# Kernel optimization log

Hardware: AMD Instinct MI355X
Metric: run time of the kernel (lower is better)

The kernel has to match this reference:

```python
import jax, jax.numpy as jnp
import numpy as np

NUM_GRAPHS = 64


def gcn_conv(x, W, b, row, col, ew, n_nodes):
    # PyG GCNConv with edge weights: add self-loops (weight 1), symmetric norm.
    deg = jax.ops.segment_sum(ew, col, num_segments=n_nodes) + 1.0  # self-loop weight
    dis = jnp.where(deg > 0, jax.lax.rsqrt(deg), 0.0)
    norm = dis[row] * ew * dis[col]  # [E]
    xw = x @ W  # [N, H]
    # edge messages aggregated at target (col) + self-loop contribution dis_i^2 * xw_i
    agg = jnp.zeros_like(xw).at[col].add(norm[:, None] * xw[row])
    agg = agg + (dis * dis)[:, None] * xw
    return agg + b


def reference(x, edge_index, edge_attr, batch, W1, b1, W2, b2, actor_w, actor_b, critic_w, critic_b):
    n_nodes = x.shape[0]
    row, col = edge_index[0], edge_index[1]
    ew = jnp.abs(edge_attr)
    h = jax.nn.relu(gcn_conv(x, W1, b1, row, col, ew, n_nodes))
    # dropout p=0.1 is identity in eval mode
    h = jax.nn.relu(gcn_conv(h, W2, b2, row, col, ew, n_nodes))
    action_logits = (h @ actor_w + actor_b)[:, 0]  # [N]
    # global mean pool over graphs
    sums = jax.ops.segment_sum(h, batch, num_segments=NUM_GRAPHS)  # [G, H]
    counts = jax.ops.segment_sum(jnp.ones((n_nodes,), h.dtype), batch, num_segments=NUM_GRAPHS)
    graph_embed = sums / jnp.maximum(counts, 1.0)[:, None]
    value = graph_embed @ critic_w + critic_b  # [G, 1]
    return (action_logits, value)


def setup_inputs() -> dict:
    key = jax.random.key(0)
    ks = jax.random.split(key, 10)
    N, F, H, E = 100000, 128, 64, 1600000
    s = lambda fan: 1.0 / np.sqrt(fan)
    return {
        "x": jax.random.normal(ks[0], (N, F), jnp.float32),
        "edge_index": jax.random.randint(ks[1], (2, E), 0, N, jnp.int32),
        "edge_attr": jax.random.normal(ks[2], (E,), jnp.float32),
        "batch": jnp.sort(jax.random.randint(ks[3], (N,), 0, 64, jnp.int32)),
        "W1": jax.random.normal(ks[4], (F, H), jnp.float32) * s(F),
        "b1": jnp.zeros((H,), jnp.float32),
        "W2": jax.random.normal(ks[5], (H, H), jnp.float32) * s(H),
        "b2": jnp.zeros((H,), jnp.float32),
        "actor_w": jax.random.normal(ks[6], (H, 1), jnp.float32) * s(H),
        "actor_b": jnp.zeros((1,), jnp.float32),
        "critic_w": jax.random.normal(ks[7], (H, 1), jnp.float32) * s(H),
        "critic_b": jnp.zeros((1,), jnp.float32),
    }
```

## Files before the change

kernel.cpp:

```cpp
#include <hip/hip_runtime.h>
#include <hip/hip_fp16.h>


#define TB 256
#define BSH2 9
#define BW2 512
#define CHUNK 4096
#define NB1MAX 256

__global__ __launch_bounds__(256) void passA_k(const int* __restrict__ col,
                                               const int* __restrict__ row,
                                               const float* __restrict__ ea,
                                               int* __restrict__ gCur,
                                               uint2* __restrict__ recA,
                                               int E, int CAPB, int NB1) {
    __shared__ int hist[NB1MAX], base[NB1MAX], cur[NB1MAX];
    int t = threadIdx.x;
    int e0 = blockIdx.x * CHUNK;
    if (t < NB1MAX) { hist[t] = 0; cur[t] = 0; }
    __syncthreads();
    for (int i = t; i < CHUNK; i += 256) {
        int e = e0 + i;
        if (e < E) atomicAdd(&hist[col[e] >> BSH2], 1);
    }
    __syncthreads();
    if (t < NB1) base[t] = atomicAdd(&gCur[t], hist[t]);
    __syncthreads();
    for (int i = t; i < CHUNK; i += 256) {
        int e = e0 + i;
        if (e >= E) continue;
        int c = col[e];
        int b = c >> BSH2;
        int pos = base[b] + atomicAdd(&cur[b], 1);
        if (pos < CAPB)
            recA[(size_t)b * CAPB + pos] =
                make_uint2(((unsigned)(c & (BW2 - 1)) << 17) | (unsigned)row[e],
                           __float_as_uint(fabsf(ea[e])));
    }
}

__global__ __launch_bounds__(256) void passB_k(const int* __restrict__ gCur,
                                               const uint2* __restrict__ recA,
                                               uint2* __restrict__ rec,
                                               int* __restrict__ ptr,
                                               int* __restrict__ cnt,
                                               float* __restrict__ dis,
                                               int N, int CAPB) {
    __shared__ int hist[BW2], excl[BW2], cur[BW2];
    __shared__ float sumL[BW2];
    __shared__ int part[256];
    int b = blockIdx.x, t = threadIdx.x;
    int nrec = min(gCur[b], CAPB);
    for (int i = t; i < BW2; i += 256) { hist[i] = 0; cur[i] = 0; sumL[i] = 0.f; }
    __syncthreads();
    const uint2* ra = recA + (size_t)b * CAPB;
    for (int i = t; i < nrec; i += 256) {
        uint2 r = ra[i];
        int lc = r.x >> 17;
        atomicAdd(&hist[lc], 1);
        atomicAdd(&sumL[lc], __uint_as_float(r.y));
    }
    __syncthreads();
    int s0 = hist[t * 2], s = s0 + hist[t * 2 + 1];
    part[t] = s;
    __syncthreads();
    for (int d = 1; d < 256; d <<= 1) {
        int v = (t >= d) ? part[t - d] : 0;
        __syncthreads();
        part[t] += v;
        __syncthreads();
    }
    int poff = t ? part[t - 1] : 0;
    excl[t * 2] = poff;
    excl[t * 2 + 1] = poff + s0;
    __syncthreads();
    for (int i = t; i < nrec; i += 256) {
        uint2 r = ra[i];
        int lc = r.x >> 17;
        int pos = atomicAdd(&cur[lc], 1);
        rec[(size_t)b * CAPB + excl[lc] + pos] = make_uint2(r.x & 0x1FFFFu, r.y);
    }
    int c0 = b << BSH2;
    for (int i = t; i < BW2; i += 256) {
        int node = c0 + i;
        if (node < N) {
            ptr[node] = b * CAPB + excl[i];
            cnt[node] = hist[i];
            dis[node] = rsqrtf(sumL[i] + 1.0f);
        }
    }
}

template <int K>
__global__ __launch_bounds__(256) void gemm_k(const float* __restrict__ X,
                                              const float* __restrict__ W,
                                              __half* __restrict__ Y, int N) {
    __shared__ float xs[16 * K];
    const int tid = threadIdx.x;
    const int row0 = blockIdx.x * 16;
    const float4* X4 = reinterpret_cast<const float4*>(X + (size_t)row0 * K);
    float4* xs4 = reinterpret_cast<float4*>(xs);
    for (int idx = tid; idx < 16 * K / 4; idx += 256) {
        int r = row0 + (idx * 4) / K;
        xs4[idx] = (r < N) ? X4[idx] : float4{0.f, 0.f, 0.f, 0.f};
    }
    __syncthreads();
    const int c  = tid & 63;
    const int rg = tid >> 6;
    const float4* xp0 = reinterpret_cast<const float4*>(xs + (rg * 4 + 0) * K);
    const float4* xp1 = reinterpret_cast<const float4*>(xs + (rg * 4 + 1) * K);
    const float4* xp2 = reinterpret_cast<const float4*>(xs + (rg * 4 + 2) * K);
    const float4* xp3 = reinterpret_cast<const float4*>(xs + (rg * 4 + 3) * K);
    float a0 = 0.f, a1 = 0.f, a2 = 0.f, a3 = 0.f;
#pragma unroll 2
    for (int k4 = 0; k4 < K / 4; ++k4) {
        float4 x0 = xp0[k4], x1 = xp1[k4], x2 = xp2[k4], x3 = xp3[k4];
        const float* wp = W + k4 * 4 * 64 + c;
        float w0 = wp[0], w1 = wp[64], w2 = wp[128], w3 = wp[192];
        a0 = fmaf(x0.x, w0, a0); a0 = fmaf(x0.y, w1, a0);
        a0 = fmaf(x0.z, w2, a0); a0 = fmaf(x0.w, w3, a0);
        a1 = fmaf(x1.x, w0, a1); a1 = fmaf(x1.y, w1, a1);
        a1 = fmaf(x1.z, w2, a1); a1 = fmaf(x1.w, w3, a1);
        a2 = fmaf(x2.x, w0, a2); a2 = fmaf(x2.y, w1, a2);
        a2 = fmaf(x2.z, w2, a2); a2 = fmaf(x2.w, w3, a2);
        a3 = fmaf(x3.x, w0, a3); a3 = fmaf(x3.y, w1, a3);
        a3 = fmaf(x3.z, w2, a3); a3 = fmaf(x3.w, w3, a3);
    }
    int r = row0 + rg * 4;
    if (r < N)     Y[(size_t)r * 64 + c]       = __float2half(a0);
    if (r + 1 < N) Y[(size_t)(r + 1) * 64 + c] = __float2half(a1);
    if (r + 2 < N) Y[(size_t)(r + 2) * 64 + c] = __float2half(a2);
    if (r + 3 < N) Y[(size_t)(r + 3) * 64 + c] = __float2half(a3);
}

__global__ __launch_bounds__(256) void agg_fin_k(const int* __restrict__ ptr,
                                                 const int* __restrict__ cnt,
                                                 const uint2* __restrict__ rec,
                                                 const float* __restrict__ dis,
                                                 const __half2* __restrict__ xw2,
                                                 const float* __restrict__ bias,
                                                 float* __restrict__ h, int N) {
    int n = blockIdx.x * 4 + (threadIdx.x >> 6);
    if (n >= N) return;
    int lane = threadIdx.x & 63;
    int half_id = lane >> 5;
    int fl = lane & 31;
    int base = ptr[n], num = cnt[n];
    float ax = 0.f, ay = 0.f;
    for (int k0 = 0; k0 < num; k0 += 64) {
        int rem = min(num - k0, 64);
        int r = 0; float w = 0.f;
        if (lane < rem) {
            uint2 rv = rec[(size_t)base + k0 + lane];
            r = (int)rv.x;
            w = __uint_as_float(rv.y) * dis[r];
        }
        int k = 0;
        for (; k + 15 < rem; k += 16) {
            int i0 = k + half_id;
            int   ra0 = __shfl(r, i0),      ra1 = __shfl(r, i0 + 2);
            int   ra2 = __shfl(r, i0 + 4),  ra3 = __shfl(r, i0 + 6);
            int   ra4 = __shfl(r, i0 + 8),  ra5 = __shfl(r, i0 + 10);
            int   ra6 = __shfl(r, i0 + 12), ra7 = __shfl(r, i0 + 14);
            float wa0 = __shfl(w, i0),      wa1 = __shfl(w, i0 + 2);
            float wa2 = __shfl(w, i0 + 4),  wa3 = __shfl(w, i0 + 6);
            float wa4 = __shfl(w, i0 + 8),  wa5 = __shfl(w, i0 + 10);
            float wa6 = __shfl(w, i0 + 12), wa7 = __shfl(w, i0 + 14);
            __half2 v0 = xw2[(size_t)ra0 * 32 + fl];
            __half2 v1 = xw2[(size_t)ra1 * 32 + fl];
            __half2 v2 = xw2[(size_t)ra2 * 32 + fl];
            __half2 v3 = xw2[(size_t)ra3 * 32 + fl];
            __half2 v4 = xw2[(size_t)ra4 * 32 + fl];
            __half2 v5 = xw2[(size_t)ra5 * 32 + fl];
            __half2 v6 = xw2[(size_t)ra6 * 32 + fl];
            __half2 v7 = xw2[(size_t)ra7 * 32 + fl];
            float2 f;
            f = __half22float2(v0); ax = fmaf(wa0, f.x, ax); ay = fmaf(wa0, f.y, ay);
            f = __half22float2(v1); ax = fmaf(wa1, f.x, ax); ay = fmaf(wa1, f.y, ay);
            f = __half22float2(v2); ax = fmaf(wa2, f.x, ax); ay = fmaf(wa2, f.y, ay);
            f = __half22float2(v3); ax = fmaf(wa3, f.x, ax); ay = fmaf(wa3, f.y, ay);
            f = __half22float2(v4); ax = fmaf(wa4, f.x, ax); ay = fmaf(wa4, f.y, ay);
            f = __half22float2(v5); ax = fmaf(wa5, f.x, ax); ay = fmaf(wa5, f.y, ay);
            f = __half22float2(v6); ax = fmaf(wa6, f.x, ax); ay = fmaf(wa6, f.y, ay);
            f = __half22float2(v7); ax = fmaf(wa7, f.x, ax); ay = fmaf(wa7, f.y, ay);
        }
        for (; k + 1 < rem; k += 2) {
            int i = k + half_id;
            int ra = __shfl(r, i); float wa = __shfl(w, i);
            float2 f = __half22float2(xw2[(size_t)ra * 32 + fl]);
            ax = fmaf(wa, f.x, ax); ay = fmaf(wa, f.y, ay);
        }
        if (k < rem) {
            int ra = __shfl(r, k); float wa = __shfl(w, k);
            if (half_id == 0) {
                float2 f = __half22float2(xw2[(size_t)ra * 32 + fl]);
                ax = fmaf(wa, f.x, ax); ay = fmaf(wa, f.y, ay);
            }
        }
    }
    ax += __shfl(ax, lane ^ 32);
    ay += __shfl(ay, lane ^ 32);
    if (half_id == 0) {
        float d = dis[n];
        float2 xs = __half22float2(xw2[(size_t)n * 32 + fl]);
        float2 bb = reinterpret_cast<const float2*>(bias)[fl];
        float svx = fmaf(d, xs.x, ax);
        float svy = fmaf(d, xs.y, ay);
        float2 out;
        out.x = fmaxf(fmaf(d, svx, bb.x), 0.0f);
        out.y = fmaxf(fmaf(d, svy, bb.y), 0.0f);
        reinterpret_cast<float2*>(h)[(size_t)n * 32 + fl] = out;
    }
}

__global__ __launch_bounds__(256) void heads_k(const float* __restrict__ h,
                                               const float* __restrict__ aw,
                                               const float* __restrict__ ab,
                                               const int* __restrict__ batch,
                                               float* __restrict__ logits,
                                               float* __restrict__ sums,
                                               float* __restrict__ counts,
                                               int N, int C) {
    int wave = blockIdx.x * 4 + (threadIdx.x >> 6);
    int lane = threadIdx.x & 63;
    int start = wave * C;
    if (start >= N) return;
    int end = min(start + C, N);
    float aww = aw[lane];
    float abv = ab[0];
    int cur = batch[start];
    float acc = 0.f;
    int cntv = 0;
    for (int i = start; i < end; ++i) {
        float hv = h[(size_t)i * 64 + lane];
        float p = hv * aww;
        for (int off = 32; off; off >>= 1) p += __shfl_down(p, off);
        if (lane == 0) logits[i] = p + abv;
        int g = batch[i];
        if (g != cur) {
            atomicAdd(&sums[cur * 64 + lane], acc);
            if (lane == 0) atomicAdd(&counts[cur], (float)cntv);
            acc = 0.f; cntv = 0; cur = g;
        }
        acc += hv; ++cntv;
    }
    atomicAdd(&sums[cur * 64 + lane], acc);
    if (lane == 0) atomicAdd(&counts[cur], (float)cntv);
}

__global__ void value_k(const float* __restrict__ sums, const float* __restrict__ counts,
                        const float* __restrict__ cw, const float* __restrict__ cb,
                        float* __restrict__ val) {
    int g = blockIdx.x;
    int lane = threadIdx.x;
    float cntv = fmaxf(counts[g], 1.0f);
    float p = (sums[g * 64 + lane] / cntv) * cw[lane];
    for (int off = 32; off; off >>= 1) p += __shfl_down(p, off);
    if (lane == 0) val[g] = p + cb[0];
}

extern "C" void kernel_launch(void* const* d_in, const int* in_sizes, int n_in,
                              void* d_out, int out_size, void* d_ws, size_t ws_size,
                              hipStream_t stream) {
    const float* x     = (const float*)d_in[0];
    const int*   ei    = (const int*)d_in[1];
    const float* ea    = (const float*)d_in[2];
    const int*   batch = (const int*)d_in[3];
    const float* W1    = (const float*)d_in[4];
    const float* b1    = (const float*)d_in[5];
    const float* W2    = (const float*)d_in[6];
    const float* b2    = (const float*)d_in[7];
    const float* aw    = (const float*)d_in[8];
    const float* ab    = (const float*)d_in[9];
    const float* cw    = (const float*)d_in[10];
    const float* cb    = (const float*)d_in[11];

    const int N = in_sizes[3];
    const int E = in_sizes[2];
    const int H = 64, G = 64;
    const int* row = ei;
    const int* col = ei + E;

    const int NB1  = (N + BW2 - 1) >> BSH2;
    const int CAPB = (((E / NB1) * 5 / 4 + 256) + 1) & ~1;

    float*  dis    = (float*)d_ws;
    int*    gCur   = (int*)(dis + N);
    uint2*  recA   = (uint2*)(gCur + NB1MAX);
    uint2*  rec    = recA + (size_t)NB1 * CAPB;
    int*    ptr    = (int*)(rec + (size_t)NB1 * CAPB);
    int*    cnt    = ptr + N;
    __half* xwh    = (__half*)(cnt + N);
    float*  bufB   = (float*)(xwh + (size_t)N * H);
    float*  sums   = bufB + (size_t)N * H;
    float*  counts = sums + G * H;

    float* logits = (float*)d_out;
    float* value  = logits + N;

    hipMemsetAsync(gCur, 0, (size_t)NB1MAX * 4, stream);
    passA_k<<<(E + CHUNK - 1) / CHUNK, 256, 0, stream>>>(col, row, ea, gCur, recA, E, CAPB, NB1);
    passB_k<<<NB1, 256, 0, stream>>>(gCur, recA, rec, ptr, cnt, dis, N, CAPB);

    gemm_k<128><<<(N + 15) / 16, 256, 0, stream>>>(x, W1, xwh, N);
    agg_fin_k<<<(N + 3) / 4, 256, 0, stream>>>(ptr, cnt, rec, dis,
                                               (const __half2*)xwh, b1, bufB, N);

    gemm_k<64><<<(N + 15) / 16, 256, 0, stream>>>(bufB, W2, xwh, N);
    agg_fin_k<<<(N + 3) / 4, 256, 0, stream>>>(ptr, cnt, rec, dis,
                                               (const __half2*)xwh, b2, bufB, N);

    hipMemsetAsync(sums, 0, (size_t)(G * H + G) * 4, stream);
    const int WAVES = 4096;
    const int C = (N + WAVES - 1) / WAVES;
    heads_k<<<WAVES / 4, 256, 0, stream>>>(bufB, aw, ab, batch, logits, sums, counts, N, C);
    value_k<<<G, 64, 0, stream>>>(sums, counts, cw, cb, value);
}
```

Before: 274.0 us.

## Store hidden activations in fp16, fuse actor logits into aggregation, merge memsets

Hidden activations between layers are now stored as fp16 instead of fp32, halving the traffic for the layer-1 output, the layer-2 GEMM input and the pooling input. The actor-head dot product is computed inside the second aggregation kernel with a wave shuffle reduction, so the separate heads kernel becomes a pooling-only kernel working on half2 data. The two memsets are merged into one by moving sums, counts and the cursor array next to each other in the workspace. Rounding hidden activations to fp16 adds precision loss, and the fused logits use fp32 values that differ slightly from the rounded values used in pooling.

```diff
diff --git a/kernel.cpp b/kernel.cpp
--- a/kernel.cpp
+++ b/kernel.cpp
@@ -91,18 +91,30 @@
     }
 }
 
-template <int K>
-__global__ __launch_bounds__(256) void gemm_k(const float* __restrict__ X,
+template <int K, typename T>
+__global__ __launch_bounds__(256) void gemm_k(const T* __restrict__ X,
                                               const float* __restrict__ W,
                                               __half* __restrict__ Y, int N) {
     __shared__ float xs[16 * K];
     const int tid = threadIdx.x;
     const int row0 = blockIdx.x * 16;
-    const float4* X4 = reinterpret_cast<const float4*>(X + (size_t)row0 * K);
     float4* xs4 = reinterpret_cast<float4*>(xs);
-    for (int idx = tid; idx < 16 * K / 4; idx += 256) {
-        int r = row0 + (idx * 4) / K;
-        xs4[idx] = (r < N) ? X4[idx] : float4{0.f, 0.f, 0.f, 0.f};
+    if constexpr (sizeof(T) == 4) {
+        const float4* X4 = reinterpret_cast<const float4*>((const float*)X + (size_t)row0 * K);
+        for (int idx = tid; idx < 16 * K / 4; idx += 256) {
+            int r = row0 + (idx * 4) / K;
+            xs4[idx] = (r < N) ? X4[idx] : float4{0.f, 0.f, 0.f, 0.f};
+        }
+    } else {
+        const __half2* X2 = reinterpret_cast<const __half2*>((const __half*)X + (size_t)row0 * K);
+        for (int idx = tid; idx < 16 * K / 4; idx += 256) {
+            int r = row0 + (idx * 4) / K;
+            if (r < N) {
+                float2 fa = __half22float2(X2[2 * idx]);
+                float2 fb = __half22float2(X2[2 * idx + 1]);
+                xs4[idx] = float4{fa.x, fa.y, fb.x, fb.y};
+            } else xs4[idx] = float4{0.f, 0.f, 0.f, 0.f};
+        }
     }
     __syncthreads();
     const int c  = tid & 63;
@@ -133,13 +145,17 @@
     if (r + 3 < N) Y[(size_t)(r + 3) * 64 + c] = __float2half(a3);
 }
 
+template <bool WITH_LOGITS>
 __global__ __launch_bounds__(256) void agg_fin_k(const int* __restrict__ ptr,
                                                  const int* __restrict__ cnt,
                                                  const uint2* __restrict__ rec,
                                                  const float* __restrict__ dis,
                                                  const __half2* __restrict__ xw2,
                                                  const float* __restrict__ bias,
-                                                 float* __restrict__ h, int N) {
+                                                 __half2* __restrict__ hout,
+                                                 const float* __restrict__ aw,
+                                                 const float* __restrict__ ab,
+                                                 float* __restrict__ logits, int N) {
     int n = blockIdx.x * 4 + (threadIdx.x >> 6);
     if (n >= N) return;
     int lane = threadIdx.x & 63;
@@ -204,48 +220,52 @@
         float d = dis[n];
         float2 xs = __half22float2(xw2[(size_t)n * 32 + fl]);
         float2 bb = reinterpret_cast<const float2*>(bias)[fl];
-        float svx = fmaf(d, xs.x, ax);
-        float svy = fmaf(d, xs.y, ay);
         float2 out;
-        out.x = fmaxf(fmaf(d, svx, bb.x), 0.0f);
-        out.y = fmaxf(fmaf(d, svy, bb.y), 0.0f);
-        reinterpret_cast<float2*>(h)[(size_t)n * 32 + fl] = out;
-    }
-}
-
-__global__ __launch_bounds__(256) void heads_k(const float* __restrict__ h,
-                                               const float* __restrict__ aw,
-                                               const float* __restrict__ ab,
-                                               const int* __restrict__ batch,
-                                               float* __restrict__ logits,
-                                               float* __restrict__ sums,
-                                               float* __restrict__ counts,
-                                               int N, int C) {
+        out.x = fmaxf(fmaf(d, fmaf(d, xs.x, ax), bb.x), 0.0f);
+        out.y = fmaxf(fmaf(d, fmaf(d, xs.y, ay), bb.y), 0.0f);
+        hout[(size_t)n * 32 + fl] = __float22half2_rn(out);
+        if constexpr (WITH_LOGITS) {
+            float2 awv = reinterpret_cast<const float2*>(aw)[fl];
+            float lg = out.x * awv.x + out.y * awv.y;
+            lg += __shfl(lg, lane ^ 1);
+            lg += __shfl(lg, lane ^ 2);
+            lg += __shfl(lg, lane ^ 4);
+            lg += __shfl(lg, lane ^ 8);
+            lg += __shfl(lg, lane ^ 16);
+            if (lane == 0) logits[n] = lg + ab[0];
+        }
+    }
+}
+
+__global__ __launch_bounds__(256) void pool_k(const __half2* __restrict__ h2,
+                                              const int* __restrict__ batch,
+                                              float* __restrict__ sums,
+                                              float* __restrict__ counts,
+                                              int N, int C) {
     int wave = blockIdx.x * 4 + (threadIdx.x >> 6);
     int lane = threadIdx.x & 63;
     int start = wave * C;
     if (start >= N) return;
+    if (lane >= 32) return;
     int end = min(start + C, N);
-    float aww = aw[lane];
-    float abv = ab[0];
+    int fl = lane;
     int cur = batch[start];
-    float acc = 0.f;
+    float accx = 0.f, accy = 0.f;
     int cntv = 0;
     for (int i = start; i < end; ++i) {
-        float hv = h[(size_t)i * 64 + lane];
-        float p = hv * aww;
-        for (int off = 32; off; off >>= 1) p += __shfl_down(p, off);
-        if (lane == 0) logits[i] = p + abv;
+        float2 v = __half22float2(h2[(size_t)i * 32 + fl]);
         int g = batch[i];
         if (g != cur) {
-            atomicAdd(&sums[cur * 64 + lane], acc);
-            if (lane == 0) atomicAdd(&counts[cur], (float)cntv);
-            acc = 0.f; cntv = 0; cur = g;
-        }
-        acc += hv; ++cntv;
-    }
-    atomicAdd(&sums[cur * 64 + lane], acc);
-    if (lane == 0) atomicAdd(&counts[cur], (float)cntv);
+            atomicAdd(&sums[cur * 64 + 2 * fl], accx);
+            atomicAdd(&sums[cur * 64 + 2 * fl + 1], accy);
+            if (fl == 0) atomicAdd(&counts[cur], (float)cntv);
+            accx = 0.f; accy = 0.f; cntv = 0; cur = g;
+        }
+        accx += v.x; accy += v.y; ++cntv;
+    }
+    atomicAdd(&sums[cur * 64 + 2 * fl], accx);
+    atomicAdd(&sums[cur * 64 + 2 * fl + 1], accy);
+    if (fl == 0) atomicAdd(&counts[cur], (float)cntv);
 }
 
 __global__ void value_k(const float* __restrict__ sums, const float* __restrict__ counts,
@@ -284,35 +304,35 @@
     const int NB1  = (N + BW2 - 1) >> BSH2;
     const int CAPB = (((E / NB1) * 5 / 4 + 256) + 1) & ~1;
 
-    float*  dis    = (float*)d_ws;
-    int*    gCur   = (int*)(dis + N);
-    uint2*  recA   = (uint2*)(gCur + NB1MAX);
+    float*  sums   = (float*)d_ws;
+    float*  counts = sums + G * H;
+    int*    gCur   = (int*)(counts + G);
+    float*  dis    = (float*)(gCur + NB1MAX);
+    uint2*  recA   = (uint2*)(dis + N);
     uint2*  rec    = recA + (size_t)NB1 * CAPB;
     int*    ptr    = (int*)(rec + (size_t)NB1 * CAPB);
     int*    cnt    = ptr + N;
     __half* xwh    = (__half*)(cnt + N);
-    float*  bufB   = (float*)(xwh + (size_t)N * H);
-    float*  sums   = bufB + (size_t)N * H;
-    float*  counts = sums + G * H;
+    __half* hbuf   = xwh + (size_t)N * H;
 
     float* logits = (float*)d_out;
     float* value  = logits + N;
 
-    hipMemsetAsync(gCur, 0, (size_t)NB1MAX * 4, stream);
+    hipMemsetAsync(sums, 0, (size_t)(G * H + G + NB1MAX) * 4, stream);
+
     passA_k<<<(E + CHUNK - 1) / CHUNK, 256, 0, stream>>>(col, row, ea, gCur, recA, E, CAPB, NB1);
     passB_k<<<NB1, 256, 0, stream>>>(gCur, recA, rec, ptr, cnt, dis, N, CAPB);
 
-    gemm_k<128><<<(N + 15) / 16, 256, 0, stream>>>(x, W1, xwh, N);
-    agg_fin_k<<<(N + 3) / 4, 256, 0, stream>>>(ptr, cnt, rec, dis,
-                                               (const __half2*)xwh, b1, bufB, N);
-
-    gemm_k<64><<<(N + 15) / 16, 256, 0, stream>>>(bufB, W2, xwh, N);
-    agg_fin_k<<<(N + 3) / 4, 256, 0, stream>>>(ptr, cnt, rec, dis,
-                                               (const __half2*)xwh, b2, bufB, N);
-
-    hipMemsetAsync(sums, 0, (size_t)(G * H + G) * 4, stream);
+    gemm_k<128, float><<<(N + 15) / 16, 256, 0, stream>>>(x, W1, xwh, N);
+    agg_fin_k<false><<<(N + 3) / 4, 256, 0, stream>>>(ptr, cnt, rec, dis,
+        (const __half2*)xwh, b1, (__half2*)hbuf, nullptr, nullptr, nullptr, N);
+
+    gemm_k<64, __half><<<(N + 15) / 16, 256, 0, stream>>>(hbuf, W2, xwh, N);
+    agg_fin_k<true><<<(N + 3) / 4, 256, 0, stream>>>(ptr, cnt, rec, dis,
+        (const __half2*)xwh, b2, (__half2*)hbuf, aw, ab, logits, N);
+
     const int WAVES = 4096;
     const int C = (N + WAVES - 1) / WAVES;
-    heads_k<<<WAVES / 4, 256, 0, stream>>>(bufB, aw, ab, batch, logits, sums, counts, N, C);
+    pool_k<<<WAVES / 4, 256, 0, stream>>>((const __half2*)hbuf, batch, sums, counts, N, C);
     value_k<<<G, 64, 0, stream>>>(sums, counts, cw, cb, value);
 }
```

New measurement: 277.6 us. No clear change (+1.3%).
